# Optimization experiments

Measured on AMD Instinct MI355X. Metric: run time of the kernel, lower is better.

The kernel has to match this reference:

```python
import jax, jax.numpy as jnp
import numpy as np

B, L, D = 2, 4096, 128      # batch, seq_len, d_model
ED = 2 * D                  # d_inner (expand=2) = 256
N = 16                      # d_state
K = 4                       # d_conv
R = (D + 15) // 16          # dt_rank = 8
H = 2 * D                   # mlp hidden = 256


def setup_inputs() -> dict:
    key = jax.random.key(0)
    ks = jax.random.split(key, 20)
    s = 0.05
    inp = {
        "x": jax.random.normal(ks[0], (B, L, D), dtype=jnp.float32),
        # outer block LayerNorm (norm1)
        "norm1_g": jnp.ones((D,), jnp.float32),
        "norm1_b": jnp.zeros((D,), jnp.float32),
        # MambaLayer inner LayerNorm
        "inner_g": jnp.ones((D,), jnp.float32),
        "inner_b": jnp.zeros((D,), jnp.float32),
        # Mamba params
        "in_w": jax.random.normal(ks[1], (2 * ED, D), jnp.float32) * s,      # in_proj (no bias)
        "conv_w": jax.random.normal(ks[2], (ED, 1, K), jnp.float32) * s,     # depthwise conv
        "conv_b": jax.random.normal(ks[3], (ED,), jnp.float32) * s,
        "xproj_w": jax.random.normal(ks[4], (R + 2 * N, ED), jnp.float32) * s,  # x_proj (no bias)
        "dt_w": jax.random.normal(ks[5], (ED, R), jnp.float32) * s,
        "dt_b": jax.random.normal(ks[6], (ED,), jnp.float32) * s,
        "A_log": jnp.tile(jnp.log(jnp.arange(1, N + 1, dtype=jnp.float32)), (ED, 1)),  # [ED,N]
        "Dp": jnp.ones((ED,), jnp.float32),
        "out_w": jax.random.normal(ks[7], (D, ED), jnp.float32) * s,         # out_proj (no bias)
        # MLP
        "fc1_w": jax.random.normal(ks[8], (H, D), jnp.float32) * s,
        "fc1_b": jnp.zeros((H,), jnp.float32),
        "fc2_w": jax.random.normal(ks[9], (D, H), jnp.float32) * s,
        "fc2_b": jnp.zeros((D,), jnp.float32),
    }
    return inp


def _ln(x, g, b, eps=1e-5):
    m = jnp.mean(x, axis=-1, keepdims=True)
    v = jnp.mean((x - m) ** 2, axis=-1, keepdims=True)
    return (x - m) * jax.lax.rsqrt(v + eps) * g + b


def _mamba(x, in_w, conv_w, conv_b, xproj_w, dt_w, dt_b, A_log, Dp, out_w):
    # x: [B, L, D]
    xz = jnp.einsum('bld,ed->ble', x, in_w)          # [B,L,2*ED]
    u, z = jnp.split(xz, 2, axis=-1)                 # each [B,L,ED]
    # causal depthwise conv1d over L
    u_c = jnp.transpose(u, (0, 2, 1))                # [B,ED,L]
    u_c = jax.lax.conv_general_dilated(
        u_c, conv_w, window_strides=(1,), padding=[(K - 1, 0)],
        dimension_numbers=('NCH', 'OIH', 'NCH'), feature_group_count=ED)
    u = jax.nn.silu(jnp.transpose(u_c, (0, 2, 1)) + conv_b)   # [B,L,ED]
    # input-dependent dt, B, C
    dbc = jnp.einsum('ble,re->blr', u, xproj_w)      # [B,L,R+2N]
    dt, Bm, Cm = jnp.split(dbc, [R, R + N], axis=-1)
    delta = jax.nn.softplus(jnp.einsum('blr,er->ble', dt, dt_w) + dt_b)  # [B,L,ED]
    A = -jnp.exp(A_log)                              # [ED,N]
    deltaA = jnp.exp(jnp.einsum('ble,en->blen', delta, A))               # [B,L,ED,N]
    deltaBu = jnp.einsum('ble,bln,ble->blen', delta, Bm, u)              # [B,L,ED,N]
    # selective scan over L
    def step(h, inp):
        dA, dBu, Ct = inp                            # [B,ED,N],[B,ED,N],[B,N]
        h = dA * h + dBu
        y = jnp.einsum('ben,bn->be', h, Ct)
        return h, y
    h0 = jnp.zeros((B, ED, N), u.dtype)
    xs = (jnp.transpose(deltaA, (1, 0, 2, 3)),
          jnp.transpose(deltaBu, (1, 0, 2, 3)),
          jnp.transpose(Cm, (1, 0, 2)))
    _, ys = jax.lax.scan(step, h0, xs)               # [L,B,ED]
    y = jnp.transpose(ys, (1, 0, 2)) + u * Dp        # [B,L,ED]
    y = y * jax.nn.silu(z)
    return jnp.einsum('ble,de->bld', y, out_w)       # [B,L,D]


def reference(x, norm1_g, norm1_b, inner_g, inner_b, in_w, conv_w, conv_b,
              xproj_w, dt_w, dt_b, A_log, Dp, out_w, fc1_w, fc1_b, fc2_w, fc2_b):
    # attn branch: mamba(inner_LN(norm1(x)))
    a = _mamba(_ln(_ln(x, norm1_g, norm1_b), inner_g, inner_b),
               in_w, conv_w, conv_b, xproj_w, dt_w, dt_b, A_log, Dp, out_w)
    x = x + a
    # mlp branch (note: original applies norm1 again to updated x)
    h = _ln(x, norm1_g, norm1_b)
    h = jax.nn.gelu(jnp.einsum('bld,hd->blh', h, fc1_w) + fc1_b, approximate=False)
    h = jnp.einsum('blh,dh->bld', h, fc2_w) + fc2_b
    return x + h
```

## Files before the change

### kernel.cpp

```cpp
#include <hip/hip_runtime.h>
#include <hip/hip_bf16.h>
#include <math.h>

#define BB 2
#define LL 4096
#define DD 128
#define ED 256
#define NN 16
#define KK 4
#define RR 8
#define HH 256
#define NT (BB*LL)
#define NC 128
#define LC 32
#define NCS 256
#define LCS 16

#define LOG2E 1.4426950408889634f
#define LN2F  0.6931471805599453f

typedef __attribute__((ext_vector_type(8))) short short8;
typedef __attribute__((ext_vector_type(8))) unsigned short ushort8v;
typedef __attribute__((ext_vector_type(4))) float floatx4;

__device__ __forceinline__ unsigned short f2bf(float f) {
  unsigned int b = __builtin_bit_cast(unsigned int, f);
  b += 0x7FFFu + ((b >> 16) & 1u);
  return (unsigned short)(b >> 16);
}

__device__ __forceinline__ float exp2_fast(float x) {
#if __has_builtin(__builtin_amdgcn_exp2f)
  return __builtin_amdgcn_exp2f(x);
#else
  return exp2f(x);
#endif
}

__device__ __forceinline__ ushort8v pack8(const float4& v0, const float4& v1) {
  ushort8v p;
  p[0]=f2bf(v0.x); p[1]=f2bf(v0.y); p[2]=f2bf(v0.z); p[3]=f2bf(v0.w);
  p[4]=f2bf(v1.x); p[5]=f2bf(v1.y); p[6]=f2bf(v1.z); p[7]=f2bf(v1.w);
  return p;
}

#define S_IN  65536
#define S_XP  10240
#define S_OUT 32768
#define S_F1  32768
#define S_F2  32768
__global__ __launch_bounds__(256) void prep_k(
    const float* __restrict__ in_w, const float* __restrict__ xpw,
    const float* __restrict__ out_w, const float* __restrict__ fc1_w,
    const float* __restrict__ fc2_w, unsigned short* __restrict__ wb) {
  const int o = (blockIdx.x*256 + threadIdx.x) * 8;
  const float* src;
  int off;
  if (o < S_IN)                          { src = in_w;  off = o; }
  else if (o < S_IN+S_XP)                { src = xpw;   off = o - S_IN; }
  else if (o < S_IN+S_XP+S_OUT)          { src = out_w; off = o - S_IN - S_XP; }
  else if (o < S_IN+S_XP+S_OUT+S_F1)     { src = fc1_w; off = o - S_IN - S_XP - S_OUT; }
  else                                   { src = fc2_w; off = o - S_IN - S_XP - S_OUT - S_F1; }
  const float4 v0 = *(const float4*)(src + off);
  const float4 v1 = *(const float4*)(src + off + 4);
  *(ushort8v*)(wb + o) = pack8(v0, v1);
}

__global__ __launch_bounds__(512, 4) void scan1n_k(
    const float* __restrict__ x,
    const float* __restrict__ g1, const float* __restrict__ b1,
    const float* __restrict__ g2, const float* __restrict__ b2,
    const unsigned short* __restrict__ wb_in,
    const float* __restrict__ cw, const float* __restrict__ cb,
    const unsigned short* __restrict__ wb_xp,
    const float* __restrict__ dtw, const float* __restrict__ dtb,
    const float* __restrict__ A_log,
    float* __restrict__ uc, float* __restrict__ dbc,
    float* __restrict__ delta, float* __restrict__ gate,
    float* __restrict__ cA, float* __restrict__ cH) {
  __shared__ __align__(16) unsigned char SM[44624];
  auto Atile = reinterpret_cast<unsigned short(*)[136]>(SM);
  auto As    = reinterpret_cast<unsigned short(*)[264]>(SM);
  auto ubuf  = reinterpret_cast<float(*)[257]>(SM + 8704);
  auto sdbc  = reinterpret_cast<float(*)[40]>(SM + 8704);
  auto sus   = reinterpret_cast<float(*)[256]>(SM + 28240);

  const int c2 = blockIdx.x, b = blockIdx.y;
  const int tid = threadIdx.x;
  const int t0 = b*LL + c2*LCS;
  const int wave = tid >> 6, lane = tid & 63;
  const int quad = lane >> 4, l16 = lane & 15;

  {
    const int lr = tid >> 4, le = (tid & 15) * 8;
    if (lr < 19 && !(c2 == 0 && lr < 3)) {
      const float* Ap = x + (size_t)(t0 - 3 + lr)*DD + le;
      float4 a0 = *(const float4*)(Ap);
      float4 a1 = *(const float4*)(Ap + 4);
      float s  = a0.x + a0.y + a0.z + a0.w + a1.x + a1.y + a1.z + a1.w;
      float sq = a0.x*a0.x + a0.y*a0.y + a0.z*a0.z + a0.w*a0.w
               + a1.x*a1.x + a1.y*a1.y + a1.z*a1.z + a1.w*a1.w;
      s += __shfl_xor(s, 1);  s += __shfl_xor(s, 2);
      s += __shfl_xor(s, 4);  s += __shfl_xor(s, 8);
      sq += __shfl_xor(sq, 1); sq += __shfl_xor(sq, 2);
      sq += __shfl_xor(sq, 4); sq += __shfl_xor(sq, 8);
      const float m1 = s * (1.f/128.f);
      const float rs1 = rsqrtf(sq*(1.f/128.f) - m1*m1 + 1e-5f);
      const float4 ga0 = *(const float4*)(g1 + le);
      const float4 ga1 = *(const float4*)(g1 + le + 4);
      const float4 bb0 = *(const float4*)(b1 + le);
      const float4 bb1 = *(const float4*)(b1 + le + 4);
      float4 v0, v1;
      v0.x = (a0.x - m1)*rs1*ga0.x + bb0.x;
      v0.y = (a0.y - m1)*rs1*ga0.y + bb0.y;
      v0.z = (a0.z - m1)*rs1*ga0.z + bb0.z;
      v0.w = (a0.w - m1)*rs1*ga0.w + bb0.w;
      v1.x = (a1.x - m1)*rs1*ga1.x + bb1.x;
      v1.y = (a1.y - m1)*rs1*ga1.y + bb1.y;
      v1.z = (a1.z - m1)*rs1*ga1.z + bb1.z;
      v1.w = (a1.w - m1)*rs1*ga1.w + bb1.w;
      float s2  = v0.x + v0.y + v0.z + v0.w + v1.x + v1.y + v1.z + v1.w;
      float sq2 = v0.x*v0.x + v0.y*v0.y + v0.z*v0.z + v0.w*v0.w
                + v1.x*v1.x + v1.y*v1.y + v1.z*v1.z + v1.w*v1.w;
      s2 += __shfl_xor(s2, 1);  s2 += __shfl_xor(s2, 2);
      s2 += __shfl_xor(s2, 4);  s2 += __shfl_xor(s2, 8);
      sq2 += __shfl_xor(sq2, 1); sq2 += __shfl_xor(sq2, 2);
      sq2 += __shfl_xor(sq2, 4); sq2 += __shfl_xor(sq2, 8);
      const float m2 = s2 * (1.f/128.f);
      const float rs2 = rsqrtf(sq2*(1.f/128.f) - m2*m2 + 1e-5f);
      const float4 gc0 = *(const float4*)(g2 + le);
      const float4 gc1 = *(const float4*)(g2 + le + 4);
      const float4 bc0 = *(const float4*)(b2 + le);
      const float4 bc1 = *(const float4*)(b2 + le + 4);
      ushort8v pa;
      pa[0] = f2bf((v0.x - m2)*rs2*gc0.x + bc0.x);
      pa[1] = f2bf((v0.y - m2)*rs2*gc0.y + bc0.y);
      pa[2] = f2bf((v0.z - m2)*rs2*gc0.z + bc0.z);
      pa[3] = f2bf((v0.w - m2)*rs2*gc0.w + bc0.w);
      pa[4] = f2bf((v1.x - m2)*rs2*gc1.x + bc1.x);
      pa[5] = f2bf((v1.y - m2)*rs2*gc1.y + bc1.y);
      pa[6] = f2bf((v1.z - m2)*rs2*gc1.z + bc1.z);
      pa[7] = f2bf((v1.w - m2)*rs2*gc1.w + bc1.w);
      *(ushort8v*)&Atile[lr][le] = pa;
    } else {
      const ushort8v zz = {};
      *(ushort8v*)&Atile[lr][le] = zz;
    }
  }
  __syncthreads();

  {
    short8 af[2][4];
    #pragma unroll
    for (int mt = 0; mt < 2; mt++)
      #pragma unroll
      for (int ks = 0; ks < 4; ks++)
        af[mt][ks] = *(const short8*)&Atile[mt*16 + l16][ks*32 + quad*8];
    const int nb = wave * 64;
    #pragma unroll
    for (int j = 0; j < 4; j++) {
      const int ncol = nb + j*16;
      floatx4 acc0 = {}, acc1 = {};
      #pragma unroll
      for (int ks = 0; ks < 4; ks++) {
        short8 bv = *(const short8*)(wb_in + (size_t)(ncol + l16)*DD + ks*32 + quad*8);
        acc0 = __builtin_amdgcn_mfma_f32_16x16x32_bf16(af[0][ks], bv, acc0, 0, 0, 0);
        acc1 = __builtin_amdgcn_mfma_f32_16x16x32_bf16(af[1][ks], bv, acc1, 0, 0, 0);
      }
      const int coll = ncol + l16;
      if (nb < 256) {
        #pragma unroll
        for (int rr = 0; rr < 4; rr++)
          ubuf[quad*4 + rr][coll] = acc0[rr];
        #pragma unroll
        for (int rr = 0; rr < 4; rr++) {
          const int m = 16 + quad*4 + rr;
          if (m < 19) ubuf[m][coll] = acc1[rr];
        }
      } else {
        const int gcol = coll - 256;
        #pragma unroll
        for (int rr = 0; rr < 4; rr++) {
          const int m = quad*4 + rr;
          if (m >= 3) {
            const float v = acc0[rr];
            gate[(size_t)(t0 + m - 3)*ED + gcol] = v / (1.f + __expf(-v));
          }
        }
        #pragma unroll
        for (int rr = 0; rr < 4; rr++) {
          const int m = 16 + quad*4 + rr;
          if (m < 19) {
            const float v = acc1[rr];
            gate[(size_t)(t0 + m - 3)*ED + gcol] = v / (1.f + __expf(-v));
          }
        }
      }
    }
  }
  __syncthreads();

  {
    const int ch = tid & 255, tg = tid >> 8;
    const int i0 = tg * 8;
    const float4 w = *(const float4*)(cw + ch*4);
    const float cbe = cb[ch];
    float v0 = ubuf[i0][ch], v1 = ubuf[i0+1][ch], v2 = ubuf[i0+2][ch];
    #pragma unroll
    for (int k = 0; k < 8; k++) {
      const float cur = ubuf[i0+3+k][ch];
      const float a = cbe + v0*w.x + v1*w.y + v2*w.z + cur*w.w;
      const float s = a / (1.f + __expf(-a));
      const int i = i0 + k;
      As[i][ch] = f2bf(s);
      sus[i][ch] = s;
      uc[(size_t)(t0+i)*ED + ch] = s;
      v0 = v1; v1 = v2; v2 = cur;
    }
  }
  __syncthreads();

  if (wave < 3) {
    const int jn = (wave == 2) ? 24 : wave*16;
    floatx4 acc = {};
    #pragma unroll
    for (int ks = 0; ks < 8; ks++) {
      const int ko = ks*32 + quad*8;
      short8 a  = *(const short8*)&As[l16][ko];
      short8 bv = *(const short8*)(wb_xp + (size_t)(jn + l16)*ED + ko);
      acc = __builtin_amdgcn_mfma_f32_16x16x32_bf16(a, bv, acc, 0, 0, 0);
    }
    const int n = jn + l16;
    if (wave < 2 || l16 >= 8) {
      #pragma unroll
      for (int rr = 0; rr < 4; rr++) {
        const int m = quad*4 + rr;
        sdbc[m][n] = acc[rr];
        dbc[(size_t)(t0 + m)*40 + n] = acc[rr];
      }
    }
  }
  __syncthreads();

  {
    const int e = tid >> 1, half = tid & 1;
    const int n0 = half * 8;
    const float4 dw0 = *(const float4*)(dtw + e*RR);
    const float4 dw1 = *(const float4*)(dtw + e*RR + 4);
    const float db = dtb[e];
    const float4 a0 = *(const float4*)(A_log + e*NN + n0);
    const float4 a1 = *(const float4*)(A_log + e*NN + n0 + 4);
    float Aen[8] = {-__expf(a0.x)*LOG2E, -__expf(a0.y)*LOG2E,
                    -__expf(a0.z)*LOG2E, -__expf(a0.w)*LOG2E,
                    -__expf(a1.x)*LOG2E, -__expf(a1.y)*LOG2E,
                    -__expf(a1.z)*LOG2E, -__expf(a1.w)*LOG2E};
    float h[8] = {};
    float sumd = 0.f;
    float4 q0 = *(const float4*)&sdbc[0][0];
    float4 q1 = *(const float4*)&sdbc[0][4];
    float4 B0 = *(const float4*)&sdbc[0][RR + n0];
    float4 B1 = *(const float4*)&sdbc[0][RR + n0 + 4];
    float su = sus[0][e];
    for (int t = 0; t < LCS; t++) {
      const float4 cq0 = q0, cq1 = q1, cB0 = B0, cB1 = B1;
      const float csu = su;
      if (t < LCS-1) {
        q0 = *(const float4*)&sdbc[t+1][0];
        q1 = *(const float4*)&sdbc[t+1][4];
        B0 = *(const float4*)&sdbc[t+1][RR + n0];
        B1 = *(const float4*)&sdbc[t+1][RR + n0 + 4];
        su = sus[t+1][e];
      }
      const float aa = db
          + cq0.x*dw0.x + cq0.y*dw0.y + cq0.z*dw0.z + cq0.w*dw0.w
          + cq1.x*dw1.x + cq1.y*dw1.y + cq1.z*dw1.z + cq1.w*dw1.w;
      float dv;
      if (aa > 20.f) dv = aa;
      else {
        const float et = exp2_fast(aa * LOG2E);
        dv = __log2f(1.f + et) * LN2F;
      }
      if (half == 0) delta[(size_t)(t0+t)*ED + e] = dv;
      const float du = dv * csu;
      const float Bv[8] = {cB0.x,cB0.y,cB0.z,cB0.w, cB1.x,cB1.y,cB1.z,cB1.w};
      sumd += dv;
      #pragma unroll
      for (int j = 0; j < 8; j++)
        h[j] = exp2_fast(dv * Aen[j])*h[j] + Bv[j]*du;
    }
    const size_t base = (((size_t)c2*BB + b)*ED + e)*NN + n0;
    *(float4*)(cA + base)     = make_float4(exp2_fast(sumd*Aen[0]), exp2_fast(sumd*Aen[1]),
                                            exp2_fast(sumd*Aen[2]), exp2_fast(sumd*Aen[3]));
    *(float4*)(cA + base + 4) = make_float4(exp2_fast(sumd*Aen[4]), exp2_fast(sumd*Aen[5]),
                                            exp2_fast(sumd*Aen[6]), exp2_fast(sumd*Aen[7]));
    *(float4*)(cH + base)     = make_float4(h[0], h[1], h[2], h[3]);
    *(float4*)(cH + base + 4) = make_float4(h[4], h[5], h[6], h[7]);
  }
}

__global__ __launch_bounds__(256) void scan2p8_k(float* __restrict__ cA,
    const float* __restrict__ cH) {
  const int gt = blockIdx.x*256 + threadIdx.x;
  const int scan = gt >> 3;
  const int seg  = gt & 7;
  const int lane = threadIdx.x & 63;
  const int lb   = lane & ~7;
  const int b = scan >> 12;
  const size_t base = (size_t)b*ED*NN + (scan & 4095);
  const int c0 = seg * 32;

  float ap = 1.f, hs = 0.f;
  for (int g = 0; g < 2; g++) {
    float av[16], hv[16];
    #pragma unroll
    for (int i = 0; i < 16; i++) {
      const size_t idx = (size_t)(c0 + g*16 + i)*(BB*ED*NN) + base;
      av[i] = cA[idx]; hv[i] = cH[idx];
    }
    #pragma unroll
    for (int i = 0; i < 16; i++) {
      hs = av[i]*hs + hv[i];
      ap *= av[i];
    }
  }
  float h = 0.f;
  #pragma unroll
  for (int k = 0; k < 7; k++) {
    const float ak = __shfl(ap, lb + k);
    const float hk = __shfl(hs, lb + k);
    if (seg > k) h = ak*h + hk;
  }
  for (int g = 0; g < 2; g++) {
    float av[16], hv[16];
    #pragma unroll
    for (int i = 0; i < 16; i++) {
      const size_t idx = (size_t)(c0 + g*16 + i)*(BB*ED*NN) + base;
      av[i] = cA[idx]; hv[i] = cH[idx];
    }
    #pragma unroll
    for (int i = 0; i < 16; i++) {
      const size_t idx = (size_t)(c0 + g*16 + i)*(BB*ED*NN) + base;
      cA[idx] = h;
      h = av[i]*h + hv[i];
    }
  }
}

__global__ __launch_bounds__(1024) void tail9_k(
    const float* __restrict__ gate, const float* __restrict__ delta,
    const float* __restrict__ uc, const float* __restrict__ dbc,
    const float* __restrict__ cP, const float* __restrict__ A_log,
    const float* __restrict__ Dpv, const float* __restrict__ x,
    const float* __restrict__ g1, const float* __restrict__ b1,
    const unsigned short* __restrict__ wb_out,
    const unsigned short* __restrict__ wb_f1,
    const unsigned short* __restrict__ wb_f2,
    const float* __restrict__ fc1_b, const float* __restrict__ fc2_b,
    float* __restrict__ out) {
  __shared__ __align__(16) unsigned short Au[32][264];
  __shared__ float xs[32][132];
  __shared__ float sbc[32][32];

  const int c = blockIdx.x, b = blockIdx.y;
  const int t0 = b*LL + c*LC;
  const int tid = threadIdx.x;
  const int wave = tid >> 6, lane = tid & 63;
  const int quad = lane >> 4, l16 = lane & 15;

  if (tid < 256) {
    const int row = tid >> 3, c4 = (tid & 7) * 4;
    *(float4*)&sbc[row][c4] = *(const float4*)(dbc + (size_t)(t0 + row)*40 + RR + c4);
  }
  __syncthreads();

  {
    const int e = tid >> 2, q = tid & 3;
    const int n0 = q * 4;
    float Aen[4], h[4];
    {
      const float4 a0 = *(const float4*)(A_log + e*NN + n0);
      Aen[0]=-__expf(a0.x)*LOG2E; Aen[1]=-__expf(a0.y)*LOG2E;
      Aen[2]=-__expf(a0.z)*LOG2E; Aen[3]=-__expf(a0.w)*LOG2E;
      const float4 h0 = *(const float4*)(cP + (((size_t)(2*c)*BB + b)*ED + e)*NN + n0);
      h[0]=h0.x; h[1]=h0.y; h[2]=h0.z; h[3]=h0.w;
    }
    const float Dpe = Dpv[e];
    float pd[8], pu[8], pg[8];
    #pragma unroll
    for (int i = 0; i < 8; i++) {
      pd[i] = delta[(size_t)(t0+i)*ED + e];
      pu[i] = uc[(size_t)(t0+i)*ED + e];
      pg[i] = gate[(size_t)(t0+i)*ED + e];
    }
    for (int g4 = 0; g4 < 4; g4++) {
      float cd[8], cu[8], cg[8];
      #pragma unroll
      for (int i = 0; i < 8; i++) { cd[i]=pd[i]; cu[i]=pu[i]; cg[i]=pg[i]; }
      if (g4 < 3) {
        const int tn = t0 + (g4+1)*8;
        #pragma unroll
        for (int i = 0; i < 8; i++) {
          pd[i] = delta[(size_t)(tn+i)*ED + e];
          pu[i] = uc[(size_t)(tn+i)*ED + e];
          pg[i] = gate[(size_t)(tn+i)*ED + e];
        }
      }
      #pragma unroll
      for (int i = 0; i < 8; i++) {
        const int t = g4*8 + i;
        const float dv = cd[i];
        const float uv = cu[i];
        const float du = dv * uv;
        const float4 B0 = *(const float4*)&sbc[t][n0];
        const float4 C0 = *(const float4*)&sbc[t][16 + n0];
        const float Bv[4] = {B0.x,B0.y,B0.z,B0.w};
        const float Cv[4] = {C0.x,C0.y,C0.z,C0.w};
        float part = 0.f;
        #pragma unroll
        for (int j = 0; j < 4; j++) {
          h[j] = exp2_fast(dv * Aen[j])*h[j] + Bv[j]*du;
          part += h[j]*Cv[j];
        }
        part += __shfl_xor(part, 1);
        part += __shfl_xor(part, 2);
        if (q == 0)
          Au[t][e] = f2bf((part + uv*Dpe) * cg[i]);
      }
    }
  }
  __syncthreads();

  {
    const int mi = (wave & 1) * 16;
    const int wn = (wave >> 1) * 16;
    floatx4 acc = {};
    #pragma unroll
    for (int ks = 0; ks < 8; ks++) {
      const int ko = ks*32 + quad*8;
      short8 a  = *(const short8*)&Au[mi + l16][ko];
      short8 bv = *(const short8*)(wb_out + (size_t)(wn + l16)*ED + ko);
      acc = __builtin_amdgcn_mfma_f32_16x16x32_bf16(a, bv, acc, 0, 0, 0);
    }
    const int n = wn + l16;
    #pragma unroll
    for (int r = 0; r < 4; r++) {
      const int m = mi + quad*4 + r;
      xs[m][n] = acc[r] + x[(size_t)(t0 + m)*DD + n];
    }
  }
  __syncthreads();

  if (tid < 512) {
    const int lr = tid >> 4, le = (tid & 15) * 8;
    float vv[8];
    float s = 0.f, sq = 0.f;
    #pragma unroll
    for (int i = 0; i < 8; i++) {
      vv[i] = xs[lr][le + i];
      s += vv[i]; sq += vv[i]*vv[i];
    }
    s += __shfl_xor(s, 1);  s += __shfl_xor(s, 2);
    s += __shfl_xor(s, 4);  s += __shfl_xor(s, 8);
    sq += __shfl_xor(sq, 1); sq += __shfl_xor(sq, 2);
    sq += __shfl_xor(sq, 4); sq += __shfl_xor(sq, 8);
    const float mean = s * (1.f/128.f);
    const float rs = rsqrtf(sq*(1.f/128.f) - mean*mean + 1e-5f);
    ushort8v p;
    #pragma unroll
    for (int i = 0; i < 8; i++)
      p[i] = f2bf((vv[i] - mean)*rs*g1[le + i] + b1[le + i]);
    *(ushort8v*)&Au[lr][le] = p;
  }
  __syncthreads();

  {
    const int mi = (wave & 1) * 16;
    const int wn = (wave >> 1) * 32;
    floatx4 acc[2] = {};
    #pragma unroll
    for (int ks = 0; ks < 4; ks++) {
      const int ko = ks*32 + quad*8;
      short8 a  = *(const short8*)&Au[mi + l16][ko];
      short8 b0 = *(const short8*)(wb_f1 + (size_t)(wn +      l16)*DD + ko);
      short8 b1v= *(const short8*)(wb_f1 + (size_t)(wn + 16 + l16)*DD + ko);
      acc[0] = __builtin_amdgcn_mfma_f32_16x16x32_bf16(a, b0, acc[0], 0, 0, 0);
      acc[1] = __builtin_amdgcn_mfma_f32_16x16x32_bf16(a, b1v, acc[1], 0, 0, 0);
    }
    __syncthreads();
    #pragma unroll
    for (int f = 0; f < 2; f++) {
      const int n = wn + f*16 + l16;
      const float bn = fc1_b[n];
      #pragma unroll
      for (int r = 0; r < 4; r++) {
        const int m = mi + quad*4 + r;
        float v = acc[f][r] + bn;
        v = 0.5f*v*(1.f + erff(v*0.70710678118f));
        Au[m][n] = f2bf(v);
      }
    }
  }
  __syncthreads();

  {
    const int mi = (wave & 1) * 16;
    const int wn = (wave >> 1) * 16;
    floatx4 acc = {};
    #pragma unroll
    for (int ks = 0; ks < 8; ks++) {
      const int ko = ks*32 + quad*8;
      short8 a  = *(const short8*)&Au[mi + l16][ko];
      short8 bv = *(const short8*)(wb_f2 + (size_t)(wn + l16)*HH + ko);
      acc = __builtin_amdgcn_mfma_f32_16x16x32_bf16(a, bv, acc, 0, 0, 0);
    }
    const int n = wn + l16;
    const float bn = fc2_b[n];
    #pragma unroll
    for (int r = 0; r < 4; r++) {
      const int m = mi + quad*4 + r;
      out[(size_t)(t0 + m)*DD + n] = acc[r] + bn + xs[m][n];
    }
  }
}

extern "C" void kernel_launch(void* const* d_in, const int* in_sizes, int n_in,
                              void* d_out, int out_size, void* d_ws, size_t ws_size,
                              hipStream_t stream) {
  const float* x      = (const float*)d_in[0];
  const float* n1g    = (const float*)d_in[1];
  const float* n1b    = (const float*)d_in[2];
  const float* ing    = (const float*)d_in[3];
  const float* inb    = (const float*)d_in[4];
  const float* in_w   = (const float*)d_in[5];
  const float* conv_w = (const float*)d_in[6];
  const float* conv_b = (const float*)d_in[7];
  const float* xproj_w= (const float*)d_in[8];
  const float* dt_w   = (const float*)d_in[9];
  const float* dt_b   = (const float*)d_in[10];
  const float* A_log  = (const float*)d_in[11];
  const float* Dpv    = (const float*)d_in[12];
  const float* out_w  = (const float*)d_in[13];
  const float* fc1_w  = (const float*)d_in[14];
  const float* fc1_b  = (const float*)d_in[15];
  const float* fc2_w  = (const float*)d_in[16];
  const float* fc2_b  = (const float*)d_in[17];
  float* out = (float*)d_out;

  float* ws    = (float*)d_ws;
  float* uc    = ws;
  float* dbc   = uc    + (size_t)NT*ED;
  float* delta = dbc   + (size_t)NT*40;
  float* gate  = delta + (size_t)NT*ED;
  float* cA    = gate  + (size_t)NT*ED;
  float* cH    = cA    + (size_t)NCS*BB*ED*NN;
  unsigned short* wb = (unsigned short*)(cH + (size_t)NCS*BB*ED*NN);
  unsigned short* wb_in  = wb;
  unsigned short* wb_xp  = wb_in  + S_IN;
  unsigned short* wb_out = wb_xp  + S_XP;
  unsigned short* wb_f1  = wb_out + S_OUT;
  unsigned short* wb_f2  = wb_f1  + S_F1;

  prep_k<<<(S_IN+S_XP+S_OUT+S_F1+S_F2)/(256*8), 256, 0, stream>>>(
      in_w, xproj_w, out_w, fc1_w, fc2_w, wb);
  scan1n_k<<<dim3(NCS, BB), 512, 0, stream>>>(x, n1g, n1b, ing, inb, wb_in,
                                              conv_w, conv_b, wb_xp, dt_w, dt_b,
                                              A_log, uc, dbc, delta, gate, cA, cH);
  scan2p8_k<<<(8*BB*ED*NN)/256, 256, 0, stream>>>(cA, cH);
  tail9_k<<<dim3(NC, BB), 1024, 0, stream>>>(gate, delta, uc, dbc, cA, A_log, Dpv,
                                             x, n1g, n1b, wb_out, wb_f1, wb_f2,
                                             fc1_b, fc2_b, out);
}
```

Measured before the change: 177.7 us.

## Split fused norm/in_proj/conv kernel into separate GEMM and conv kernels

Splits the first fused kernel into two. gemmA_k computes the double LayerNorm and the in_proj GEMM for 16 tokens and writes u and the gated z to global memory. convB_k then reads u from global for the causal conv and runs the rest of the old pipeline. This removes the 3-token halo recompute (19 rows padded to 32, giving two MFMA M-tiles) and cuts shared memory per block, which may raise occupancy. In exchange it adds a full global round trip of u (NT*256 floats), an extra kernel launch and a larger workspace.

```diff
diff --git a/kernel.cpp b/kernel.cpp
--- a/kernel.cpp
+++ b/kernel.cpp
@@ -21,6 +21,7 @@
 
 typedef __attribute__((ext_vector_type(8))) short short8;
 typedef __attribute__((ext_vector_type(8))) unsigned short ushort8v;
+typedef __attribute__((ext_vector_type(4))) unsigned short ushort4v;
 typedef __attribute__((ext_vector_type(4))) float floatx4;
 
 __device__ __forceinline__ unsigned short f2bf(float f) {
@@ -66,24 +67,100 @@
   *(ushort8v*)(wb + o) = pack8(v0, v1);
 }
 
-__global__ __launch_bounds__(512, 4) void scan1n_k(
+__global__ __launch_bounds__(512, 4) void gemmA_k(
     const float* __restrict__ x,
     const float* __restrict__ g1, const float* __restrict__ b1,
     const float* __restrict__ g2, const float* __restrict__ b2,
     const unsigned short* __restrict__ wb_in,
+    float* __restrict__ u, float* __restrict__ gate) {
+  __shared__ __align__(16) unsigned short Atile[16][136];
+  const int c2 = blockIdx.x, b = blockIdx.y;
+  const int tid = threadIdx.x;
+  const int t0 = b*LL + c2*LCS;
+  const int wave = tid >> 6, lane = tid & 63;
+  const int quad = lane >> 4, l16 = lane & 15;
+
+  {
+    const int lr = tid >> 5, le = (tid & 31) * 4;
+    const float* Ap = x + (size_t)(t0 + lr)*DD + le;
+    const float4 a0 = *(const float4*)(Ap);
+    float s  = a0.x + a0.y + a0.z + a0.w;
+    float sq = a0.x*a0.x + a0.y*a0.y + a0.z*a0.z + a0.w*a0.w;
+    s += __shfl_xor(s, 1);  s += __shfl_xor(s, 2);
+    s += __shfl_xor(s, 4);  s += __shfl_xor(s, 8);  s += __shfl_xor(s, 16);
+    sq += __shfl_xor(sq, 1); sq += __shfl_xor(sq, 2);
+    sq += __shfl_xor(sq, 4); sq += __shfl_xor(sq, 8); sq += __shfl_xor(sq, 16);
+    const float m1 = s * (1.f/128.f);
+    const float rs1 = rsqrtf(sq*(1.f/128.f) - m1*m1 + 1e-5f);
+    const float4 ga = *(const float4*)(g1 + le);
+    const float4 ba = *(const float4*)(b1 + le);
+    float4 v;
+    v.x = (a0.x - m1)*rs1*ga.x + ba.x;
+    v.y = (a0.y - m1)*rs1*ga.y + ba.y;
+    v.z = (a0.z - m1)*rs1*ga.z + ba.z;
+    v.w = (a0.w - m1)*rs1*ga.w + ba.w;
+    float s2  = v.x + v.y + v.z + v.w;
+    float sq2 = v.x*v.x + v.y*v.y + v.z*v.z + v.w*v.w;
+    s2 += __shfl_xor(s2, 1);  s2 += __shfl_xor(s2, 2);
+    s2 += __shfl_xor(s2, 4);  s2 += __shfl_xor(s2, 8);  s2 += __shfl_xor(s2, 16);
+    sq2 += __shfl_xor(sq2, 1); sq2 += __shfl_xor(sq2, 2);
+    sq2 += __shfl_xor(sq2, 4); sq2 += __shfl_xor(sq2, 8); sq2 += __shfl_xor(sq2, 16);
+    const float m2 = s2 * (1.f/128.f);
+    const float rs2 = rsqrtf(sq2*(1.f/128.f) - m2*m2 + 1e-5f);
+    const float4 gc = *(const float4*)(g2 + le);
+    const float4 bc = *(const float4*)(b2 + le);
+    ushort4v p;
+    p[0] = f2bf((v.x - m2)*rs2*gc.x + bc.x);
+    p[1] = f2bf((v.y - m2)*rs2*gc.y + bc.y);
+    p[2] = f2bf((v.z - m2)*rs2*gc.z + bc.z);
+    p[3] = f2bf((v.w - m2)*rs2*gc.w + bc.w);
+    *(ushort4v*)&Atile[lr][le] = p;
+  }
+  __syncthreads();
+
+  {
+    short8 af[4];
+    #pragma unroll
+    for (int ks = 0; ks < 4; ks++)
+      af[ks] = *(const short8*)&Atile[l16][ks*32 + quad*8];
+    const int nb = wave * 64;
+    #pragma unroll
+    for (int j = 0; j < 4; j++) {
+      const int ncol = nb + j*16;
+      floatx4 acc = {};
+      #pragma unroll
+      for (int ks = 0; ks < 4; ks++) {
+        short8 bv = *(const short8*)(wb_in + (size_t)(ncol + l16)*DD + ks*32 + quad*8);
+        acc = __builtin_amdgcn_mfma_f32_16x16x32_bf16(af[ks], bv, acc, 0, 0, 0);
+      }
+      const int coll = ncol + l16;
+      if (nb < 256) {
+        #pragma unroll
+        for (int rr = 0; rr < 4; rr++)
+          u[(size_t)(t0 + quad*4 + rr)*ED + coll] = acc[rr];
+      } else {
+        #pragma unroll
+        for (int rr = 0; rr < 4; rr++) {
+          const float v = acc[rr];
+          gate[(size_t)(t0 + quad*4 + rr)*ED + coll - 256] = v / (1.f + __expf(-v));
+        }
+      }
+    }
+  }
+}
+
+__global__ __launch_bounds__(512, 4) void convB_k(
+    const float* __restrict__ u,
     const float* __restrict__ cw, const float* __restrict__ cb,
     const unsigned short* __restrict__ wb_xp,
     const float* __restrict__ dtw, const float* __restrict__ dtb,
     const float* __restrict__ A_log,
     float* __restrict__ uc, float* __restrict__ dbc,
-    float* __restrict__ delta, float* __restrict__ gate,
+    float* __restrict__ delta,
     float* __restrict__ cA, float* __restrict__ cH) {
-  __shared__ __align__(16) unsigned char SM[44624];
-  auto Atile = reinterpret_cast<unsigned short(*)[136]>(SM);
-  auto As    = reinterpret_cast<unsigned short(*)[264]>(SM);
-  auto ubuf  = reinterpret_cast<float(*)[257]>(SM + 8704);
-  auto sdbc  = reinterpret_cast<float(*)[40]>(SM + 8704);
-  auto sus   = reinterpret_cast<float(*)[256]>(SM + 28240);
+  __shared__ __align__(16) unsigned short As[16][264];
+  __shared__ float sus[16][256];
+  __shared__ float sdbc[16][40];
 
   const int c2 = blockIdx.x, b = blockIdx.y;
   const int tid = threadIdx.x;
@@ -92,123 +169,20 @@
   const int quad = lane >> 4, l16 = lane & 15;
 
   {
-    const int lr = tid >> 4, le = (tid & 15) * 8;
-    if (lr < 19 && !(c2 == 0 && lr < 3)) {
-      const float* Ap = x + (size_t)(t0 - 3 + lr)*DD + le;
-      float4 a0 = *(const float4*)(Ap);
-      float4 a1 = *(const float4*)(Ap + 4);
-      float s  = a0.x + a0.y + a0.z + a0.w + a1.x + a1.y + a1.z + a1.w;
-      float sq = a0.x*a0.x + a0.y*a0.y + a0.z*a0.z + a0.w*a0.w
-               + a1.x*a1.x + a1.y*a1.y + a1.z*a1.z + a1.w*a1.w;
-      s += __shfl_xor(s, 1);  s += __shfl_xor(s, 2);
-      s += __shfl_xor(s, 4);  s += __shfl_xor(s, 8);
-      sq += __shfl_xor(sq, 1); sq += __shfl_xor(sq, 2);
-      sq += __shfl_xor(sq, 4); sq += __shfl_xor(sq, 8);
-      const float m1 = s * (1.f/128.f);
-      const float rs1 = rsqrtf(sq*(1.f/128.f) - m1*m1 + 1e-5f);
-      const float4 ga0 = *(const float4*)(g1 + le);
-      const float4 ga1 = *(const float4*)(g1 + le + 4);
-      const float4 bb0 = *(const float4*)(b1 + le);
-      const float4 bb1 = *(const float4*)(b1 + le + 4);
-      float4 v0, v1;
-      v0.x = (a0.x - m1)*rs1*ga0.x + bb0.x;
-      v0.y = (a0.y - m1)*rs1*ga0.y + bb0.y;
-      v0.z = (a0.z - m1)*rs1*ga0.z + bb0.z;
-      v0.w = (a0.w - m1)*rs1*ga0.w + bb0.w;
-      v1.x = (a1.x - m1)*rs1*ga1.x + bb1.x;
-      v1.y = (a1.y - m1)*rs1*ga1.y + bb1.y;
-      v1.z = (a1.z - m1)*rs1*ga1.z + bb1.z;
-      v1.w = (a1.w - m1)*rs1*ga1.w + bb1.w;
-      float s2  = v0.x + v0.y + v0.z + v0.w + v1.x + v1.y + v1.z + v1.w;
-      float sq2 = v0.x*v0.x + v0.y*v0.y + v0.z*v0.z + v0.w*v0.w
-                + v1.x*v1.x + v1.y*v1.y + v1.z*v1.z + v1.w*v1.w;
-      s2 += __shfl_xor(s2, 1);  s2 += __shfl_xor(s2, 2);
-      s2 += __shfl_xor(s2, 4);  s2 += __shfl_xor(s2, 8);
-      sq2 += __shfl_xor(sq2, 1); sq2 += __shfl_xor(sq2, 2);
-      sq2 += __shfl_xor(sq2, 4); sq2 += __shfl_xor(sq2, 8);
-      const float m2 = s2 * (1.f/128.f);
-      const float rs2 = rsqrtf(sq2*(1.f/128.f) - m2*m2 + 1e-5f);
-      const float4 gc0 = *(const float4*)(g2 + le);
-      const float4 gc1 = *(const float4*)(g2 + le + 4);
-      const float4 bc0 = *(const float4*)(b2 + le);
-      const float4 bc1 = *(const float4*)(b2 + le + 4);
-      ushort8v pa;
-      pa[0] = f2bf((v0.x - m2)*rs2*gc0.x + bc0.x);
-      pa[1] = f2bf((v0.y - m2)*rs2*gc0.y + bc0.y);
-      pa[2] = f2bf((v0.z - m2)*rs2*gc0.z + bc0.z);
-      pa[3] = f2bf((v0.w - m2)*rs2*gc0.w + bc0.w);
-      pa[4] = f2bf((v1.x - m2)*rs2*gc1.x + bc1.x);
-      pa[5] = f2bf((v1.y - m2)*rs2*gc1.y + bc1.y);
-      pa[6] = f2bf((v1.z - m2)*rs2*gc1.z + bc1.z);
-      pa[7] = f2bf((v1.w - m2)*rs2*gc1.w + bc1.w);
-      *(ushort8v*)&Atile[lr][le] = pa;
-    } else {
-      const ushort8v zz = {};
-      *(ushort8v*)&Atile[lr][le] = zz;
-    }
-  }
-  __syncthreads();
-
-  {
-    short8 af[2][4];
-    #pragma unroll
-    for (int mt = 0; mt < 2; mt++)
-      #pragma unroll
-      for (int ks = 0; ks < 4; ks++)
-        af[mt][ks] = *(const short8*)&Atile[mt*16 + l16][ks*32 + quad*8];
-    const int nb = wave * 64;
-    #pragma unroll
-    for (int j = 0; j < 4; j++) {
-      const int ncol = nb + j*16;
-      floatx4 acc0 = {}, acc1 = {};
-      #pragma unroll
-      for (int ks = 0; ks < 4; ks++) {
-        short8 bv = *(const short8*)(wb_in + (size_t)(ncol + l16)*DD + ks*32 + quad*8);
-        acc0 = __builtin_amdgcn_mfma_f32_16x16x32_bf16(af[0][ks], bv, acc0, 0, 0, 0);
-        acc1 = __builtin_amdgcn_mfma_f32_16x16x32_bf16(af[1][ks], bv, acc1, 0, 0, 0);
-      }
-      const int coll = ncol + l16;
-      if (nb < 256) {
-        #pragma unroll
-        for (int rr = 0; rr < 4; rr++)
-          ubuf[quad*4 + rr][coll] = acc0[rr];
-        #pragma unroll
-        for (int rr = 0; rr < 4; rr++) {
-          const int m = 16 + quad*4 + rr;
-          if (m < 19) ubuf[m][coll] = acc1[rr];
-        }
-      } else {
-        const int gcol = coll - 256;
-        #pragma unroll
-        for (int rr = 0; rr < 4; rr++) {
-          const int m = quad*4 + rr;
-          if (m >= 3) {
-            const float v = acc0[rr];
-            gate[(size_t)(t0 + m - 3)*ED + gcol] = v / (1.f + __expf(-v));
-          }
-        }
-        #pragma unroll
-        for (int rr = 0; rr < 4; rr++) {
-          const int m = 16 + quad*4 + rr;
-          if (m < 19) {
-            const float v = acc1[rr];
-            gate[(size_t)(t0 + m - 3)*ED + gcol] = v / (1.f + __expf(-v));
-          }
-        }
-      }
-    }
-  }
-  __syncthreads();
-
-  {
     const int ch = tid & 255, tg = tid >> 8;
     const int i0 = tg * 8;
     const float4 w = *(const float4*)(cw + ch*4);
     const float cbe = cb[ch];
-    float v0 = ubuf[i0][ch], v1 = ubuf[i0+1][ch], v2 = ubuf[i0+2][ch];
+    float v0, v1, v2;
+    if (c2 == 0 && tg == 0) { v0 = 0.f; v1 = 0.f; v2 = 0.f; }
+    else {
+      v0 = u[(size_t)(t0+i0-3)*ED + ch];
+      v1 = u[(size_t)(t0+i0-2)*ED + ch];
+      v2 = u[(size_t)(t0+i0-1)*ED + ch];
+    }
     #pragma unroll
     for (int k = 0; k < 8; k++) {
-      const float cur = ubuf[i0+3+k][ch];
+      const float cur = u[(size_t)(t0+i0+k)*ED + ch];
       const float a = cbe + v0*w.x + v1*w.y + v2*w.z + cur*w.w;
       const float s = a / (1.f + __expf(-a));
       const int i = i0 + k;
@@ -547,7 +521,8 @@
   float* out = (float*)d_out;
 
   float* ws    = (float*)d_ws;
-  float* uc    = ws;
+  float* u     = ws;
+  float* uc    = u     + (size_t)NT*ED;
   float* dbc   = uc    + (size_t)NT*ED;
   float* delta = dbc   + (size_t)NT*40;
   float* gate  = delta + (size_t)NT*ED;
@@ -562,9 +537,11 @@
 
   prep_k<<<(S_IN+S_XP+S_OUT+S_F1+S_F2)/(256*8), 256, 0, stream>>>(
       in_w, xproj_w, out_w, fc1_w, fc2_w, wb);
-  scan1n_k<<<dim3(NCS, BB), 512, 0, stream>>>(x, n1g, n1b, ing, inb, wb_in,
-                                              conv_w, conv_b, wb_xp, dt_w, dt_b,
-                                              A_log, uc, dbc, delta, gate, cA, cH);
+  gemmA_k<<<dim3(NCS, BB), 512, 0, stream>>>(x, n1g, n1b, ing, inb, wb_in,
+                                             u, gate);
+  convB_k<<<dim3(NCS, BB), 512, 0, stream>>>(u, conv_w, conv_b, wb_xp,
+                                             dt_w, dt_b, A_log,
+                                             uc, dbc, delta, cA, cH);
   scan2p8_k<<<(8*BB*ED*NN)/256, 256, 0, stream>>>(cA, cH);
   tail9_k<<<dim3(NC, BB), 1024, 0, stream>>>(gate, delta, uc, dbc, cA, A_log, Dpv,
                                              x, n1g, n1b, wb_out, wb_f1, wb_f2,
```

Result: no change. 178.3 us (+0.4%).
